# Kernel optimization log

Hardware: AMD Instinct MI355X
Metric: run time of the kernel (lower is better)

## Reference

```python
import jax, jax.numpy as jnp
import numpy as np

B, S, D_IN, D_OUT = 4, 2048, 1024, 1024

def setup_inputs() -> dict:
    key = jax.random.key(0)
    k1, k2, k3, k4 = jax.random.split(key, 4)
    sc = 0.02
    return {
        "x": jax.random.normal(k1, (B, S, D_IN), dtype=jnp.float32),
        "Wq": jax.random.normal(k2, (D_OUT, D_IN), dtype=jnp.float32) * sc,
        "Wk": jax.random.normal(k3, (D_OUT, D_IN), dtype=jnp.float32) * sc,
        "Wv": jax.random.normal(k4, (D_OUT, D_IN), dtype=jnp.float32) * sc,
    }

def reference(x, Wq, Wk, Wv):
    # torch Linear: y = x @ W.T  (weights stored [out, in])
    b, n, _ = x.shape
    q = jnp.einsum('bnd,od->bno', x, Wq)  # [B,S,D_OUT]
    k = jnp.einsum('bnd,od->bno', x, Wk)
    v = jnp.einsum('bnd,od->bno', x, Wv)
    scores = jnp.einsum('bqd,bkd->bqk', q, k)  # [B,S,S]
    # causal mask: positions j > i masked to -inf BEFORE scaling (matches source)
    causal = jnp.triu(jnp.ones((n, n), dtype=bool), k=1)
    scores = jnp.where(causal[None, :, :], -jnp.inf, scores)
    scale = 1.0 / jnp.sqrt(jnp.float32(k.shape[-1]))
    attn = jax.nn.softmax(scores * scale, axis=-1)
    # NOTE: source calls dropout but discards its output -> no-op
    return jnp.einsum('bqk,bkd->bqd', attn, v)
```

## Files before the change

### kernel.cpp

```cpp
#include <hip/hip_runtime.h>
#include <hip/hip_bf16.h>
#include <hip/hip_fp16.h>


using bf16 = __hip_bfloat16;
typedef __bf16 bf16x8 __attribute__((ext_vector_type(8)));
typedef float f32x4 __attribute__((ext_vector_type(4)));

__device__ __forceinline__ void load_lds_16B(const void* g, void* l) {
  __builtin_amdgcn_global_load_lds(
      (const __attribute__((address_space(1))) unsigned int*)g,
      (__attribute__((address_space(3))) unsigned int*)l, 16, 0, 0);
}

template <int N>
__device__ __forceinline__ void waitcnt_vm() {
  if constexpr (N == 10) asm volatile("s_waitcnt vmcnt(10)" ::: "memory");
  else if constexpr (N == 8) asm volatile("s_waitcnt vmcnt(8)" ::: "memory");
  else if constexpr (N == 6) asm volatile("s_waitcnt vmcnt(6)" ::: "memory");
  else if constexpr (N == 5) asm volatile("s_waitcnt vmcnt(5)" ::: "memory");
  else asm volatile("s_waitcnt vmcnt(0)" ::: "memory");
}

__device__ __forceinline__ int swz(int o) { return o ^ (((o >> 7) & 7) << 4); }

template <int BM, int BN, int WM, int WN, int STHR, int OCC, int OUT,
          bool CSKIP, bool KLIM, int NPASS>
__global__ __launch_bounds__(WM* WN * 64, OCC) void gemmT(
    const bf16* __restrict__ A, const bf16* __restrict__ Bm, void* __restrict__ Cv,
    int K, int lda, int ldb, int ldc, long sAz, long sBz, long sCzBytes,
    const float* __restrict__ invs) {
  constexpr int MR = BM / WM / 16, NR = BN / WN / 16, MH2 = MR / 2;
  constexpr int AKC = BM * 64;
  constexpr int BKC = BN * 64;
  constexpr int DBSTR = 2 * (AKC + BKC);
  constexpr int CHUNK = STHR * 16;
  constexpr int ACALLS = AKC / CHUNK;
  constexpr int BCALLS = BKC / CHUNK;
  constexpr int VM_LEAVE = ACALLS + 2 * BCALLS;

  const int tn = blockIdx.x, z = blockIdx.z;
  if (CSKIP && (long)tn * BN >= (long)blockIdx.y * BM + BM) return;
  A += (long)z * sAz;
  Bm += (long)z * sBz;
  char* C = (char*)Cv + (long)z * sCzBytes;
  const float* invz = invs ? (invs + (long)z * 2048) : nullptr;

  __shared__ __align__(128) char sm[2 * DBSTR];
  const int tid = threadIdx.x, lane = tid & 63, wv = tid >> 6;
  const int wr = wv / WN, wc = wv % WN;
  const int ldsw = wv * 1024;
  const int ts = (tid < STHR) ? tid : 0;

  int aoff[MR], boff[NR];
#pragma unroll
  for (int m = 0; m < MR; m++)
    aoff[m] = swz((wr * (BM / WM) + m * 16 + (lane & 15)) * 64 + (lane >> 4) * 16);
#pragma unroll
  for (int n = 0; n < NR; n++)
    boff[n] = 2 * AKC + swz((wc * (BN / WN) + n * 16 + (lane & 15)) * 64 + (lane >> 4) * 16);

  const char* srcB[BCALLS];
#pragma unroll
  for (int c = 0; c < BCALLS; c++) {
    int os = swz(c * CHUNK + ts * 16);
    srcB[c] = (const char*)(Bm + ((long)tn * BN + (os >> 6)) * ldb) + (os & 63);
  }

  for (int pass = 0; pass < NPASS; ++pass) {
    const int tm = (NPASS == 2)
                       ? (pass == 0 ? blockIdx.y : 2 * (int)gridDim.y - 1 - (int)blockIdx.y)
                       : (int)blockIdx.y;

    int kEnd = K;
    if (KLIM) kEnd = min(tm * BM + BM, K);
    int nt = kEnd >> 6;
    if (KLIM) nt = (nt + 1) & ~1;
    const int NI = nt >> 1;

    const char* srcA[ACALLS];
#pragma unroll
    for (int c = 0; c < ACALLS; c++) {
      int os = swz(c * CHUNK + ts * 16);
      srcA[c] = (const char*)(A + ((long)tm * BM + (os >> 6)) * lda) + (os & 63);
    }
    auto stageA = [&](int t, int kc) {
      if (tid < STHR) {
#pragma unroll
        for (int c = 0; c < ACALLS; c++)
          load_lds_16B(srcA[c] + (long)t * 128 + kc * 64,
                       sm + (t & 1) * DBSTR + kc * AKC + c * CHUNK + ldsw);
      }
    };
    auto stageB = [&](int t, int kc) {
      if (tid < STHR) {
#pragma unroll
        for (int c = 0; c < BCALLS; c++)
          load_lds_16B(srcB[c] + (long)t * 128 + kc * 64,
                       sm + (t & 1) * DBSTR + 2 * AKC + kc * BKC + c * CHUNK + ldsw);
      }
    };

    f32x4 acc[MR][NR] = {};
    bf16x8 bfr[2][NR];
    bf16x8 afrA[MH2], afrB[MH2];

#define LDB(DBUF, KC)                                                          \
  _Pragma("unroll") for (int n = 0; n < NR; n++)                               \
      bfr[KC][n] = *(const bf16x8*)(sm + (DBUF)*DBSTR + (KC)*BKC + boff[n]);
#define LDA(DBUF, KC, MH, DST)                                                 \
  _Pragma("unroll") for (int m = 0; m < MH2; m++)                              \
      DST[m] = *(const bf16x8*)(sm + (DBUF)*DBSTR + (KC)*AKC + aoff[(MH)*MH2 + m]);
#define MFMAS(KC, MH, AFR)                                                     \
  __builtin_amdgcn_s_setprio(1);                                               \
  _Pragma("unroll") for (int m = 0; m < MH2; m++)                              \
      _Pragma("unroll") for (int n = 0; n < NR; n++)                           \
          acc[(MH)*MH2 + m][n] = __builtin_amdgcn_mfma_f32_16x16x32_bf16(      \
              AFR[m], bfr[KC][n], acc[(MH)*MH2 + m][n], 0, 0, 0);              \
  __builtin_amdgcn_s_setprio(0);
#define BAR1()                                                                 \
  __builtin_amdgcn_s_barrier();                                                \
  asm volatile("s_waitcnt lgkmcnt(0)" ::: "memory");                           \
  __builtin_amdgcn_sched_barrier(0);
#define BAR2() __builtin_amdgcn_s_barrier();

    stageB(0, 0); stageA(0, 0); stageB(0, 1); stageA(0, 1);
    stageB(1, 0); stageA(1, 0); stageB(1, 1);
    waitcnt_vm<VM_LEAVE>();
    __builtin_amdgcn_s_barrier();

    for (int i = 0; i < NI - 1; i++) {
      const int ta = 2 * i, tb = 2 * i + 1;
      LDB(0, 0); LDA(0, 0, 0, afrA); stageA(tb, 1);     BAR1(); MFMAS(0, 0, afrA); BAR2();
      LDA(0, 0, 1, afrB);            stageB(ta + 2, 0); BAR1(); MFMAS(0, 1, afrB); BAR2();
      LDB(0, 1); LDA(0, 1, 0, afrA); stageA(ta + 2, 0); BAR1(); MFMAS(1, 0, afrA); BAR2();
      LDA(0, 1, 1, afrB);            stageB(ta + 2, 1);
      waitcnt_vm<VM_LEAVE>();                           BAR1(); MFMAS(1, 1, afrB); BAR2();
      LDB(1, 0); LDA(1, 0, 0, afrA); stageA(ta + 2, 1); BAR1(); MFMAS(0, 0, afrA); BAR2();
      LDA(1, 0, 1, afrB);            stageB(tb + 2, 0); BAR1(); MFMAS(0, 1, afrB); BAR2();
      LDB(1, 1); LDA(1, 1, 0, afrA); stageA(tb + 2, 0); BAR1(); MFMAS(1, 0, afrA); BAR2();
      LDA(1, 1, 1, afrB);            stageB(tb + 2, 1);
      waitcnt_vm<VM_LEAVE>();                           BAR1(); MFMAS(1, 1, afrB); BAR2();
    }
    {
      const int tb = nt - 1;
      LDB(0, 0); LDA(0, 0, 0, afrA); stageA(tb, 1); BAR1(); MFMAS(0, 0, afrA); BAR2();
      LDA(0, 0, 1, afrB);                           BAR1(); MFMAS(0, 1, afrB); BAR2();
      LDB(0, 1); LDA(0, 1, 0, afrA);                BAR1(); MFMAS(1, 0, afrA); BAR2();
      LDA(0, 1, 1, afrB); waitcnt_vm<0>();          BAR1(); MFMAS(1, 1, afrB); BAR2();
      LDB(1, 0); LDA(1, 0, 0, afrA);                BAR1(); MFMAS(0, 0, afrA); BAR2();
      LDA(1, 0, 1, afrB);                           BAR1(); MFMAS(0, 1, afrB); BAR2();
      LDB(1, 1); LDA(1, 1, 0, afrA);                BAR1(); MFMAS(1, 0, afrA); BAR2();
      LDA(1, 1, 1, afrB);                           BAR1(); MFMAS(1, 1, afrB); BAR2();
    }
#undef LDB
#undef LDA
#undef MFMAS
#undef BAR1
#undef BAR2

    const int cr0 = tm * BM + wr * (BM / WM) + (lane >> 4) * 4;
    const int cc0 = tn * BN + wc * (BN / WN) + (lane & 15);
#pragma unroll
    for (int m = 0; m < MR; m++)
#pragma unroll
      for (int n = 0; n < NR; n++)
#pragma unroll
        for (int j = 0; j < 4; j++) {
          long row = cr0 + m * 16 + j;
          long col = cc0 + n * 16;
          if (OUT == 1) {
            ((bf16*)C)[row * (long)ldc + col] = __float2bfloat16(acc[m][n][j]);
          } else if (OUT == 3) {
            float e = (col <= row) ? __expf(acc[m][n][j] * 0.03125f) : 0.f;
            ((bf16*)C)[row * (long)ldc + col] = __float2bfloat16(e);
          } else if (OUT == 4) {
            ((float*)C)[row * (long)ldc + col] = acc[m][n][j] * invz[row];
          } else {
            ((float*)C)[row * (long)ldc + col] = acc[m][n][j];
          }
        }
  }
}

__global__ __launch_bounds__(256) void cvt_all(const float* __restrict__ x,
                                               const float* __restrict__ wq,
                                               const float* __restrict__ wk,
                                               const float* __restrict__ wv,
                                               bf16* __restrict__ xb,
                                               bf16* __restrict__ wb) {
  const int b = blockIdx.x;
  const float* src;
  bf16* dst;
  int i;
  if (b < 8192) { src = x; dst = xb; i = b * 256 + threadIdx.x; }
  else if (b < 9216) { src = wq; dst = wb; i = (b - 8192) * 256 + threadIdx.x; }
  else if (b < 10240) { src = wk; dst = wb + 1048576; i = (b - 9216) * 256 + threadIdx.x; }
  else { src = wv; dst = wb + 2097152; i = (b - 10240) * 256 + threadIdx.x; }
  float4 f = ((const float4*)src)[i];
  union { bf16 h[4]; uint2 u; } o;
  o.h[0] = __float2bfloat16(f.x);
  o.h[1] = __float2bfloat16(f.y);
  o.h[2] = __float2bfloat16(f.z);
  o.h[3] = __float2bfloat16(f.w);
  ((uint2*)dst)[i] = o.u;
}

__global__ __launch_bounds__(256) void rowsum_inv(const bf16* __restrict__ E,
                                                  float* __restrict__ invs) {
  const int i = blockIdx.x, b = blockIdx.y;
  const bf16* row = E + ((long)b * 2048 + i) * 2048;
  const int tid = threadIdx.x, lane = tid & 63, wv = tid >> 6;
  const int len = i + 1;
  const int j0 = tid * 8;

  float s = 0.f;
  if (j0 < len) {
    union { bf16 h[8]; uint4 u4; } u;
    u.u4 = *(const uint4*)(row + j0);
#pragma unroll
    for (int e = 0; e < 8; e++)
      if (j0 + e < len) s += __bfloat162float(u.h[e]);
  }
  for (int o = 32; o; o >>= 1) s += __shfl_xor(s, o);
  __shared__ float reds[4];
  if (lane == 0) reds[wv] = s;
  __syncthreads();
  if (tid == 0) {
    s = reds[0] + reds[1] + reds[2] + reds[3];
    invs[(long)b * 2048 + i] = 1.0f / s;
  }
}

__global__ __launch_bounds__(256) void transposeV(const bf16* __restrict__ V,
                                                  bf16* __restrict__ Vt) {
  __shared__ bf16 t[32][33];
  const int b = blockIdx.z;
  const int s0 = blockIdx.x << 5;
  const int d0 = blockIdx.y << 5;
  const bf16* Vb = V + (long)b * 2048 * 3072;
  bf16* Vtb = Vt + (long)b * 1024 * 2048;
  const int lx = threadIdx.x & 31, ly = threadIdx.x >> 5;
#pragma unroll
  for (int r = 0; r < 32; r += 8)
    t[r + ly][lx] = Vb[(long)(s0 + r + ly) * 3072 + d0 + lx];
  __syncthreads();
#pragma unroll
  for (int r = 0; r < 32; r += 8)
    Vtb[(long)(d0 + r + ly) * 2048 + s0 + lx] = t[lx][r + ly];
}

extern "C" void kernel_launch(void* const* d_in, const int* in_sizes, int n_in,
                              void* d_out, int out_size, void* d_ws, size_t ws_size,
                              hipStream_t stream) {
  const float* x = (const float*)d_in[0];
  const float* Wq = (const float*)d_in[1];
  const float* Wk = (const float*)d_in[2];
  const float* Wv = (const float*)d_in[3];

  const long MBy = 1 << 20;
  char* ws = (char*)d_ws;
  bf16* Cqkv = (bf16*)(ws);
  bf16* Vt = (bf16*)(ws + 48 * MBy);
  bf16* E = (bf16*)(ws + 64 * MBy);
  float* invs = (float*)(ws + 96 * MBy);
  bf16* xb = (bf16*)(ws + 97 * MBy);
  bf16* Wb = (bf16*)(ws + 115 * MBy);

  cvt_all<<<11264, 256, 0, stream>>>(x, Wq, Wk, Wv, xb, Wb);

  gemmT<256, 192, 2, 4, 256, 2, 1, false, false, 1><<<dim3(16, 32), 512, 0, stream>>>(
      xb, Wb, Cqkv, 1024, 1024, 1024, 3072, 0L, 0L, 0L, nullptr);

  transposeV<<<dim3(64, 32, 4), 256, 0, stream>>>(Cqkv + 2048, Vt);

  gemmT<128, 128, 2, 2, 256, 2, 3, true, false, 1><<<dim3(16, 16, 4), 256, 0, stream>>>(
      Cqkv, Cqkv + 1024, E, 1024, 3072, 3072, 2048,
      2048L * 3072, 2048L * 3072, 2048L * 2048 * 2, nullptr);

  rowsum_inv<<<dim3(2048, 4), 256, 0, stream>>>(E, invs);

  gemmT<128, 128, 2, 2, 256, 2, 4, false, true, 2><<<dim3(8, 8, 4), 256, 0, stream>>>(
      E, Vt, d_out, 2048, 2048, 2048, 1024,
      2048L * 2048, 1024L * 2048, 2048L * 1024 * 4, invs);
}
```

Baseline: 162.6 us.

## Fuse V transpose and softmax row-sums into GEMM epilogues

The QKV projection epilogue now writes V directly in transposed layout, which removes the separate transpose kernel. The score GEMM epilogue reduces each row's exp values with shuffles and atomically adds them into a row-sum buffer, which removes the rowsum kernel. That buffer is zeroed by extra blocks in the conversion kernel. This saves two launches and a full re-read of E, but adds strided scattered stores for V^T and atomic traffic, and the row sums are now taken in fp32 before bf16 rounding.

```diff
diff --git a/kernel.cpp b/kernel.cpp
--- a/kernel.cpp
+++ b/kernel.cpp
@@ -29,7 +29,7 @@
 __global__ __launch_bounds__(WM* WN * 64, OCC) void gemmT(
     const bf16* __restrict__ A, const bf16* __restrict__ Bm, void* __restrict__ Cv,
     int K, int lda, int ldb, int ldc, long sAz, long sBz, long sCzBytes,
-    const float* __restrict__ invs) {
+    void* __restrict__ aux) {
   constexpr int MR = BM / WM / 16, NR = BN / WN / 16, MH2 = MR / 2;
   constexpr int AKC = BM * 64;
   constexpr int BKC = BN * 64;
@@ -44,7 +44,6 @@
   A += (long)z * sAz;
   Bm += (long)z * sBz;
   char* C = (char*)Cv + (long)z * sCzBytes;
-  const float* invz = invs ? (invs + (long)z * 2048) : nullptr;
 
   __shared__ __align__(128) char sm[2 * DBSTR];
   const int tid = threadIdx.x, lane = tid & 63, wv = tid >> 6;
@@ -161,25 +160,64 @@
 
     const int cr0 = tm * BM + wr * (BM / WM) + (lane >> 4) * 4;
     const int cc0 = tn * BN + wc * (BN / WN) + (lane & 15);
-#pragma unroll
-    for (int m = 0; m < MR; m++)
-#pragma unroll
-      for (int n = 0; n < NR; n++)
-#pragma unroll
-        for (int j = 0; j < 4; j++) {
-          long row = cr0 + m * 16 + j;
-          long col = cc0 + n * 16;
-          if (OUT == 1) {
-            ((bf16*)C)[row * (long)ldc + col] = __float2bfloat16(acc[m][n][j]);
-          } else if (OUT == 3) {
+
+    if (OUT == 3) {
+      float* sums = (float*)aux + (long)z * 2048;
+#pragma unroll
+      for (int m = 0; m < MR; m++) {
+        float rs[4] = {0.f, 0.f, 0.f, 0.f};
+#pragma unroll
+        for (int n = 0; n < NR; n++)
+#pragma unroll
+          for (int j = 0; j < 4; j++) {
+            long row = cr0 + m * 16 + j;
+            long col = cc0 + n * 16;
             float e = (col <= row) ? __expf(acc[m][n][j] * 0.03125f) : 0.f;
             ((bf16*)C)[row * (long)ldc + col] = __float2bfloat16(e);
-          } else if (OUT == 4) {
-            ((float*)C)[row * (long)ldc + col] = acc[m][n][j] * invz[row];
-          } else {
-            ((float*)C)[row * (long)ldc + col] = acc[m][n][j];
+            rs[j] += e;
           }
+#pragma unroll
+        for (int o = 1; o < 16; o <<= 1) {
+#pragma unroll
+          for (int j = 0; j < 4; j++) rs[j] += __shfl_xor(rs[j], o);
         }
+        if ((lane & 15) == 0) {
+#pragma unroll
+          for (int j = 0; j < 4; j++)
+            atomicAdd(&sums[cr0 + m * 16 + j], rs[j]);
+        }
+      }
+    } else {
+#pragma unroll
+      for (int m = 0; m < MR; m++) {
+        float inv[4];
+        if (OUT == 4) {
+          const float* sums = (const float*)aux + (long)z * 2048;
+#pragma unroll
+          for (int j = 0; j < 4; j++) inv[j] = 1.0f / sums[cr0 + m * 16 + j];
+        }
+#pragma unroll
+        for (int n = 0; n < NR; n++)
+#pragma unroll
+          for (int j = 0; j < 4; j++) {
+            long row = cr0 + m * 16 + j;
+            long col = cc0 + n * 16;
+            if (OUT == 5) {
+              bf16 v = __float2bfloat16(acc[m][n][j]);
+              if (col < 2048) {
+                ((bf16*)C)[row * (long)ldc + col] = v;
+              } else {
+                long b = row >> 11, s = row & 2047, d = col - 2048;
+                ((bf16*)aux)[((b << 10) + d) * 2048 + s] = v;
+              }
+            } else if (OUT == 4) {
+              ((float*)C)[row * (long)ldc + col] = acc[m][n][j] * inv[j];
+            } else {
+              ((float*)C)[row * (long)ldc + col] = acc[m][n][j];
+            }
+          }
+      }
+    }
   }
 }
 
@@ -188,8 +226,13 @@
                                                const float* __restrict__ wk,
                                                const float* __restrict__ wv,
                                                bf16* __restrict__ xb,
-                                               bf16* __restrict__ wb) {
+                                               bf16* __restrict__ wb,
+                                               float* __restrict__ sums) {
   const int b = blockIdx.x;
+  if (b >= 11264) {
+    ((float4*)sums)[(b - 11264) * 256 + threadIdx.x] = float4{0.f, 0.f, 0.f, 0.f};
+    return;
+  }
   const float* src;
   bf16* dst;
   int i;
@@ -206,50 +249,6 @@
   ((uint2*)dst)[i] = o.u;
 }
 
-__global__ __launch_bounds__(256) void rowsum_inv(const bf16* __restrict__ E,
-                                                  float* __restrict__ invs) {
-  const int i = blockIdx.x, b = blockIdx.y;
-  const bf16* row = E + ((long)b * 2048 + i) * 2048;
-  const int tid = threadIdx.x, lane = tid & 63, wv = tid >> 6;
-  const int len = i + 1;
-  const int j0 = tid * 8;
-
-  float s = 0.f;
-  if (j0 < len) {
-    union { bf16 h[8]; uint4 u4; } u;
-    u.u4 = *(const uint4*)(row + j0);
-#pragma unroll
-    for (int e = 0; e < 8; e++)
-      if (j0 + e < len) s += __bfloat162float(u.h[e]);
-  }
-  for (int o = 32; o; o >>= 1) s += __shfl_xor(s, o);
-  __shared__ float reds[4];
-  if (lane == 0) reds[wv] = s;
-  __syncthreads();
-  if (tid == 0) {
-    s = reds[0] + reds[1] + reds[2] + reds[3];
-    invs[(long)b * 2048 + i] = 1.0f / s;
-  }
-}
-
-__global__ __launch_bounds__(256) void transposeV(const bf16* __restrict__ V,
-                                                  bf16* __restrict__ Vt) {
-  __shared__ bf16 t[32][33];
-  const int b = blockIdx.z;
-  const int s0 = blockIdx.x << 5;
-  const int d0 = blockIdx.y << 5;
-  const bf16* Vb = V + (long)b * 2048 * 3072;
-  bf16* Vtb = Vt + (long)b * 1024 * 2048;
-  const int lx = threadIdx.x & 31, ly = threadIdx.x >> 5;
-#pragma unroll
-  for (int r = 0; r < 32; r += 8)
-    t[r + ly][lx] = Vb[(long)(s0 + r + ly) * 3072 + d0 + lx];
-  __syncthreads();
-#pragma unroll
-  for (int r = 0; r < 32; r += 8)
-    Vtb[(long)(d0 + r + ly) * 2048 + s0 + lx] = t[lx][r + ly];
-}
-
 extern "C" void kernel_launch(void* const* d_in, const int* in_sizes, int n_in,
                               void* d_out, int out_size, void* d_ws, size_t ws_size,
                               hipStream_t stream) {
@@ -263,24 +262,20 @@
   bf16* Cqkv = (bf16*)(ws);
   bf16* Vt = (bf16*)(ws + 48 * MBy);
   bf16* E = (bf16*)(ws + 64 * MBy);
-  float* invs = (float*)(ws + 96 * MBy);
+  float* sums = (float*)(ws + 96 * MBy);
   bf16* xb = (bf16*)(ws + 97 * MBy);
   bf16* Wb = (bf16*)(ws + 115 * MBy);
 
-  cvt_all<<<11264, 256, 0, stream>>>(x, Wq, Wk, Wv, xb, Wb);
-
-  gemmT<256, 192, 2, 4, 256, 2, 1, false, false, 1><<<dim3(16, 32), 512, 0, stream>>>(
-      xb, Wb, Cqkv, 1024, 1024, 1024, 3072, 0L, 0L, 0L, nullptr);
-
-  transposeV<<<dim3(64, 32, 4), 256, 0, stream>>>(Cqkv + 2048, Vt);
+  cvt_all<<<11272, 256, 0, stream>>>(x, Wq, Wk, Wv, xb, Wb, sums);
+
+  gemmT<256, 192, 2, 4, 256, 2, 5, false, false, 1><<<dim3(16, 32), 512, 0, stream>>>(
+      xb, Wb, Cqkv, 1024, 1024, 1024, 3072, 0L, 0L, 0L, Vt);
 
   gemmT<128, 128, 2, 2, 256, 2, 3, true, false, 1><<<dim3(16, 16, 4), 256, 0, stream>>>(
       Cqkv, Cqkv + 1024, E, 1024, 3072, 3072, 2048,
-      2048L * 3072, 2048L * 3072, 2048L * 2048 * 2, nullptr);
-
-  rowsum_inv<<<dim3(2048, 4), 256, 0, stream>>>(E, invs);
+      2048L * 3072, 2048L * 3072, 2048L * 2048 * 2, sums);
 
   gemmT<128, 128, 2, 2, 256, 2, 4, false, true, 2><<<dim3(8, 8, 4), 256, 0, stream>>>(
       E, Vt, d_out, 2048, 2048, 2048, 1024,
-      2048L * 2048, 1024L * 2048, 2048L * 1024 * 4, invs);
-}
+      2048L * 2048, 1024L * 2048, 2048L * 1024 * 4, sums);
+}
```

After: 179.6 us. 10.5% more time.
